# Optimization experiments

Hardware: AMD Instinct MI355X
Metric: run time of the kernel (lower is better)

## Reference

```python
import jax, jax.numpy as jnp
import numpy as np

B, T, H, W = 4, 32, 160, 320
NF, FPF = 8, 8          # num_filters, features_per_filter
SPEED_DIM = 8           # speed_embedding output width
U = 64                  # internal LTC neurons (wiring units)
S = NF * FPF + SPEED_DIM  # 72 sensory inputs
M = 1                   # motor (output) neurons
ODE_UNFOLDS = 6
EPS = 1e-8


def setup_inputs() -> dict:
    key = jax.random.key(0)
    k = jax.random.split(key, 20)
    f32 = jnp.float32
    sp = (H // 8) * (W // 8)  # spatial size per filter after 3 stride-2 convs = 800
    d = {}
    d["input_sequence"] = jax.random.normal(k[0], (B, T, 3, H, W), f32)
    d["speed_sequence"] = jax.random.uniform(k[1], (B, T, 1), f32)
    # conv head params
    d["conv1_w"] = jax.random.normal(k[2], (16, 3, 5, 5), f32) * 0.05
    d["conv1_b"] = jnp.zeros((16,), f32)
    d["conv2_w"] = jax.random.normal(k[3], (32, 16, 5, 5), f32) * 0.05
    d["conv2_b"] = jnp.zeros((32,), f32)
    d["conv3_w"] = jax.random.normal(k[4], (NF, 32, 5, 5), f32) * 0.05
    d["conv3_b"] = jnp.zeros((NF,), f32)
    d["head_w"] = jax.random.normal(k[5], (NF, sp, FPF), f32) * 0.02  # per-filter Linear
    d["head_b"] = jnp.zeros((NF, FPF), f32)
    # speed embedding MLP (Dropout is identity at inference)
    d["se_w1"] = jax.random.normal(k[6], (1, 16), f32) * 0.5
    d["se_b1"] = jnp.zeros((16,), f32)
    d["se_w2"] = jax.random.normal(k[7], (16, SPEED_DIM), f32) * 0.3
    d["se_b2"] = jnp.zeros((SPEED_DIM,), f32)
    # LTC cell params (ncps-style init ranges)
    d["input_w"] = jnp.ones((S,), f32)
    d["input_b"] = jnp.zeros((S,), f32)
    d["gleak"] = jax.random.uniform(k[8], (U,), f32, 0.001, 1.0)
    d["vleak"] = jax.random.uniform(k[9], (U,), f32, -0.2, 0.2)
    d["cm"] = jax.random.uniform(k[10], (U,), f32, 0.4, 0.6)
    d["sigma"] = jax.random.uniform(k[11], (U, U), f32, 3.0, 8.0)
    d["mu"] = jax.random.uniform(k[12], (U, U), f32, 0.3, 0.8)
    d["w_syn"] = jax.random.uniform(k[13], (U, U), f32, 0.001, 1.0)
    d["erev"] = jnp.asarray(jax.random.bernoulli(k[14], 0.5, (U, U)), f32) * 2.0 - 1.0
    d["sensory_sigma"] = jax.random.uniform(k[15], (S, U), f32, 3.0, 8.0)
    d["sensory_mu"] = jax.random.uniform(k[16], (S, U), f32, 0.3, 0.8)
    d["sensory_w"] = jax.random.uniform(k[17], (S, U), f32, 0.001, 1.0)
    d["sensory_erev"] = jnp.asarray(jax.random.bernoulli(k[18], 0.5, (S, U)), f32) * 2.0 - 1.0
    d["output_w"] = jnp.ones((M,), f32)
    d["output_b"] = jnp.zeros((M,), f32)
    return d


def _conv(x, w, b, stride):
    y = jax.lax.conv_general_dilated(
        x, w, (stride, stride), [(2, 2), (2, 2)],
        dimension_numbers=("NCHW", "OIHW", "NCHW"))
    return jax.nn.relu(y + b[None, :, None, None])


def reference(input_sequence, speed_sequence, conv1_w, conv1_b, conv2_w, conv2_b,
              conv3_w, conv3_b, head_w, head_b, se_w1, se_b1, se_w2, se_b2,
              input_w, input_b, gleak, vleak, cm, sigma, mu, w_syn, erev,
              sensory_sigma, sensory_mu, sensory_w, sensory_erev, output_w, output_b):
    Bv, Tv = input_sequence.shape[:2]
    # ---- conv head over all frames at once ----
    x = input_sequence.reshape(Bv * Tv, 3, H, W)
    x = _conv(x, conv1_w, conv1_b, 2)
    x = _conv(x, conv2_w, conv2_b, 2)
    x = _conv(x, conv3_w, conv3_b, 2)          # [N, NF, H/8, W/8]
    x = x.reshape(Bv * Tv, NF, -1)             # [N, NF, 800]
    feats = jnp.einsum("nfp,fpk->nfk", x, head_w) + head_b  # per-filter Linear
    feats = feats.reshape(Bv, Tv, NF * FPF)    # [B, T, 64]
    # global-std normalization (torch .std() uses ddof=1)
    feats = feats / (jnp.std(feats, ddof=1) + 1e-5)
    # ---- speed embedding (vectorized over B,T) ----
    s = speed_sequence[..., :1]                # [B, T, 1]
    emb = jnp.tanh(jax.nn.relu(s @ se_w1 + se_b1) @ se_w2 + se_b2)  # [B, T, 8]
    xs = jnp.concatenate([feats, emb], axis=-1)   # [B, T, S]
    xs = jnp.swapaxes(xs, 0, 1)                   # [T, B, S]
    cm_t = cm * ODE_UNFOLDS  # cm / (elapsed_time / ode_unfolds), elapsed_time = 1.0

    def step(v, x_t):
        inp = x_t * input_w + input_b  # affine input mapping, [B, S]
        s_act = sensory_w * jax.nn.sigmoid((inp[:, :, None] - sensory_mu) * sensory_sigma)  # [B,S,U]
        w_num_s = jnp.sum(s_act * sensory_erev, axis=1)
        w_den_s = jnp.sum(s_act, axis=1)
        for _ in range(ODE_UNFOLDS):  # semi-implicit Euler unfolds
            w_act = w_syn * jax.nn.sigmoid((v[:, :, None] - mu) * sigma)  # [B,U,U]
            w_num = jnp.sum(w_act * erev, axis=1) + w_num_s
            w_den = jnp.sum(w_act, axis=1) + w_den_s
            v = (cm_t * v + gleak * vleak + w_num) / (cm_t + gleak + w_den + EPS)
        out = v[:, :M] * output_w + output_b  # affine output mapping on motor neurons
        return v, (out, v)

    v0 = jnp.zeros((Bv, U), feats.dtype)
    v_last, (outs, hs) = jax.lax.scan(step, v0, xs)
    readout = jnp.swapaxes(outs, 0, 1)  # [B, T, M]
    all_h = jnp.swapaxes(hs, 0, 1)      # [B, T, U]
    return readout, v_last, all_h
```

## Files before the change

kernel.cpp:

```cpp
#include <hip/hip_runtime.h>
#include <math.h>

#define BB 4
#define TT 32
#define NF 8
#define FPF 8
#define SDIM 8
#define UU 64
#define SS 72
#define UNFOLDS 6

typedef short short8 __attribute__((ext_vector_type(8)));
typedef float f32x4 __attribute__((ext_vector_type(4)));
union Frag { uint4 u; short8 s; };

__device__ __forceinline__ float fast_sigmoid(float x) {
    float e = exp2f(-1.44269504f * x);
    return __builtin_amdgcn_rcpf(1.0f + e);
}

__device__ __forceinline__ ushort f2b(float f) {
    union { float f; uint u; } a;
    a.f = f;
    uint u = a.u;
    return (ushort)((u + 0x7FFFu + ((u >> 16) & 1u)) >> 16);
}

__device__ __forceinline__ float bcast_lane(float v, int lane) {
    return __uint_as_float(__builtin_amdgcn_readlane(__float_as_uint(v), lane));
}

__device__ __forceinline__ void cvt_body(const float* __restrict__ in,
                                         ushort* __restrict__ outp, int idx) {
    int x = idx % 320;
    int r = idx / 320;
    int y = r % 160;
    int n = r / 160;
    const float* base = in + ((size_t)n * 3 * 160 + y) * 320 + x;
    float c0 = base[0];
    float c1 = base[160 * 320];
    float c2 = base[2 * 160 * 320];
    uint2 pk;
    pk.x = (uint)f2b(c0) | ((uint)f2b(c1) << 16);
    pk.y = (uint)f2b(c2);
    *(uint2*)(outp + ((size_t)((n * 164 + y + 2) * 328) + (x + 2)) * 4) = pk;
}

template <int HP, int WP, int H, int W, int CH>
__device__ __forceinline__ void halo_body(ushort* __restrict__ buf, int bid) {
    constexpr int TOPBOT = 2 * WP;
    constexpr int SIDE = WP - W;
    constexpr int NH = 2 * TOPBOT + H * SIDE;
    int idx = bid * 256 + threadIdx.x;
    if (idx >= 128 * NH) return;
    int n = idx / NH;
    int h = idx - n * NH;
    int y, x;
    if (h < TOPBOT) {
        y = h / WP;
        x = h % WP;
    } else if (h < 2 * TOPBOT) {
        int hh = h - TOPBOT;
        y = H + 2 + hh / WP;
        x = hh % WP;
    } else {
        int hh = h - 2 * TOPBOT;
        y = 2 + hh / SIDE;
        int xi = hh % SIDE;
        x = (xi < 2) ? xi : (W + xi);
    }
    ushort* p = buf + (((size_t)n * HP + y) * WP + x) * CH;
    if constexpr (CH == 4) {
        *(uint2*)p = make_uint2(0u, 0u);
    } else {
        uint4 z = make_uint4(0u, 0u, 0u, 0u);
#pragma unroll
        for (int i = 0; i < CH / 8; i++) *(uint4*)(p + i * 8) = z;
    }
}

__device__ __forceinline__ uint4 pack8(const ushort v[8]) {
    uint4 u;
    u.x = (uint)v[0] | ((uint)v[1] << 16);
    u.y = (uint)v[2] | ((uint)v[3] << 16);
    u.z = (uint)v[4] | ((uint)v[5] << 16);
    u.w = (uint)v[6] | ((uint)v[7] << 16);
    return u;
}

__device__ __forceinline__ void wswz1_body(const float* __restrict__ w, uint4* __restrict__ o,
                                           int i) {
    int lane = i & 63, s = i >> 6;
    int oc = lane & 15, q = lane >> 4;
    ushort v[8];
#pragma unroll
    for (int j = 0; j < 8; j++) {
        int k = q * 8 + j;
        int kx = k >> 2, c = k & 3;
        float f = (kx < 5 && c < 3) ? w[((oc * 3 + c) * 5 + s) * 5 + kx] : 0.f;
        v[j] = f2b(f);
    }
    o[i] = pack8(v);
}
__device__ __forceinline__ void wswz2_body(const float* __restrict__ w, uint4* __restrict__ o,
                                           int i) {
    int lane = i & 63;
    int ct = (i >> 6) & 1;
    int s = i >> 7;
    int ky = s / 3, kxp = s % 3;
    int oc = ct * 16 + (lane & 15);
    int q = lane >> 4, h = q >> 1;
    int kx = 2 * kxp + h;
    ushort v[8];
#pragma unroll
    for (int j = 0; j < 8; j++) {
        int ch = (q & 1) * 8 + j;
        float f = (kx < 5) ? w[((oc * 16 + ch) * 5 + ky) * 5 + kx] : 0.f;
        v[j] = f2b(f);
    }
    o[i] = pack8(v);
}
__device__ __forceinline__ void wswz3_body(const float* __restrict__ w, uint4* __restrict__ o,
                                           int i) {
    int lane = i & 63, s = i >> 6;
    int ky = s / 5, kx = s % 5;
    int oc = lane & 15, q = lane >> 4;
    ushort v[8];
#pragma unroll
    for (int j = 0; j < 8; j++) {
        int ch = q * 8 + j;
        float f = (oc < 8) ? w[((oc * 32 + ch) * 5 + ky) * 5 + kx] : 0.f;
        v[j] = f2b(f);
    }
    o[i] = pack8(v);
}

__global__ __launch_bounds__(256) void prep_kernel(
    const float* __restrict__ in_seq, ushort* __restrict__ inp1, ushort* __restrict__ c1out,
    ushort* __restrict__ c2out, const float* __restrict__ c1w, const float* __restrict__ c2w,
    const float* __restrict__ c3w, uint4* __restrict__ wz1, uint4* __restrict__ wz2,
    uint4* __restrict__ wz3) {
    int bid = blockIdx.x;
    if (bid < 25600) {
        cvt_body(in_seq, inp1, bid * 256 + threadIdx.x);
    } else if (bid < 25600 + 2032) {
        int hb = bid - 25600;
        if (hb < 1296)
            halo_body<164, 328, 160, 320, 4>(inp1, hb);
        else if (hb < 1296 + 488)
            halo_body<84, 164, 80, 160, 16>(c1out, hb - 1296);
        else
            halo_body<44, 84, 40, 80, 32>(c2out, hb - 1784);
    } else {
        int i = (bid - 27632) * 256 + threadIdx.x;
        if (i < 320)
            wswz1_body(c1w, wz1, i);
        else if (i < 2240)
            wswz2_body(c2w, wz2, i - 320);
        else
            wswz3_body(c3w, wz3, i - 2240);
    }
}

__global__ __launch_bounds__(256) void conv1_mfma(const ushort* __restrict__ inp,
                                                  const uint4* __restrict__ wswz,
                                                  const float* __restrict__ bias,
                                                  ushort* __restrict__ outp) {
    const int lane = threadIdx.x & 63;
    const int wid = threadIdx.x >> 6;
    const int col = lane & 15, q = lane >> 4;

    Frag A[5];
#pragma unroll
    for (int s = 0; s < 5; s++) A[s].u = wswz[s * 64 + lane];
    float b0 = bias[q * 4 + 0], b1 = bias[q * 4 + 1], b2 = bias[q * 4 + 2], b3 = bias[q * 4 + 3];

    int gw = blockIdx.x * 4 + wid;
#pragma unroll
    for (int t = 0; t < 4; t++) {
        int p0 = gw * 64 + t * 16;
        int n = p0 / 12800;
        int rem = p0 - n * 12800;
        int oy = rem / 160;
        int ox0 = rem - oy * 160;
        int ox = ox0 + col;
        uint e0 = ((uint)(n * 164 + oy * 2) * 328u + (uint)(ox * 2 + 2 * q)) * 4u;
        f32x4 acc = {0.f, 0.f, 0.f, 0.f};
#pragma unroll
        for (int s = 0; s < 5; s++) {
            Frag B;
            B.u = *(const uint4*)(inp + e0 + (uint)s * (328u * 4u));
            acc = __builtin_amdgcn_mfma_f32_16x16x32_bf16(A[s].s, B.s, acc, 0, 0, 0);
        }
        uint oe = ((uint)(n * 84 + oy + 2) * 164u + (uint)(ox + 2)) * 16u + q * 4u;
        uint2 pk;
        pk.x = (uint)f2b(fmaxf(acc[0] + b0, 0.f)) | ((uint)f2b(fmaxf(acc[1] + b1, 0.f)) << 16);
        pk.y = (uint)f2b(fmaxf(acc[2] + b2, 0.f)) | ((uint)f2b(fmaxf(acc[3] + b3, 0.f)) << 16);
        *(uint2*)(outp + oe) = pk;
    }
}

__global__ __launch_bounds__(256) void conv2_mfma(const ushort* __restrict__ inp,
                                                  const uint4* __restrict__ wswz,
                                                  const float* __restrict__ bias,
                                                  ushort* __restrict__ outp) {
    const int lane = threadIdx.x & 63;
    const int wid = threadIdx.x >> 6;
    const int col = lane & 15, q = lane >> 4;
    const int h = q >> 1, chh = q & 1;

    int gw = blockIdx.x * 4 + wid;
    uint eb[4];
#pragma unroll
    for (int t = 0; t < 4; t++) {
        int p0 = gw * 64 + t * 16;
        int n = p0 / 3200;
        int rem = p0 - n * 3200;
        int oy = rem / 80;
        int ox0 = rem - oy * 80;
        eb[t] = ((uint)(n * 84 + oy * 2) * 164u + (uint)((ox0 + col) * 2 + h)) * 16u + chh * 8u;
    }
    f32x4 acc[4][2];
#pragma unroll
    for (int t = 0; t < 4; t++) {
        acc[t][0] = {0.f, 0.f, 0.f, 0.f};
        acc[t][1] = {0.f, 0.f, 0.f, 0.f};
    }
#pragma unroll
    for (int s = 0; s < 15; s++) {
        const int ky = s / 3, kxp = s % 3;
        Frag A0, A1;
        A0.u = wswz[(s * 2 + 0) * 64 + lane];
        A1.u = wswz[(s * 2 + 1) * 64 + lane];
        const uint d = (uint)ky * (164u * 16u) + (uint)kxp * 32u;
#pragma unroll
        for (int t = 0; t < 4; t++) {
            Frag B;
            B.u = *(const uint4*)(inp + eb[t] + d);
            acc[t][0] = __builtin_amdgcn_mfma_f32_16x16x32_bf16(A0.s, B.s, acc[t][0], 0, 0, 0);
            acc[t][1] = __builtin_amdgcn_mfma_f32_16x16x32_bf16(A1.s, B.s, acc[t][1], 0, 0, 0);
        }
    }
    float ba[2][4];
#pragma unroll
    for (int c = 0; c < 2; c++)
#pragma unroll
        for (int r = 0; r < 4; r++) ba[c][r] = bias[c * 16 + q * 4 + r];
#pragma unroll
    for (int t = 0; t < 4; t++) {
        int p0 = gw * 64 + t * 16;
        int n = p0 / 3200;
        int rem = p0 - n * 3200;
        int oy = rem / 80;
        int ox0 = rem - oy * 80;
        int ox = ox0 + col;
        uint oe = ((uint)(n * 44 + oy + 2) * 84u + (uint)(ox + 2)) * 32u;
#pragma unroll
        for (int c = 0; c < 2; c++) {
            uint2 pk;
            pk.x = (uint)f2b(fmaxf(acc[t][c][0] + ba[c][0], 0.f)) |
                   ((uint)f2b(fmaxf(acc[t][c][1] + ba[c][1], 0.f)) << 16);
            pk.y = (uint)f2b(fmaxf(acc[t][c][2] + ba[c][2], 0.f)) |
                   ((uint)f2b(fmaxf(acc[t][c][3] + ba[c][3], 0.f)) << 16);
            *(uint2*)(outp + oe + (uint)c * 16u + (uint)q * 4u) = pk;
        }
    }
}

__global__ __launch_bounds__(256) void conv3_mfma(const ushort* __restrict__ inp,
                                                  const uint4* __restrict__ wswz,
                                                  const float* __restrict__ bias,
                                                  float* __restrict__ outp) {
    const int lane = threadIdx.x & 63;
    const int wid = threadIdx.x >> 6;
    const int col = lane & 15, q = lane >> 4;

    int gw = blockIdx.x * 4 + wid;
    uint eb[4];
#pragma unroll
    for (int t = 0; t < 4; t++) {
        int p0 = gw * 64 + t * 16;
        int n = p0 / 800;
        int pix = p0 - n * 800 + col;
        int oy = pix / 40;
        int ox = pix - oy * 40;
        eb[t] = ((uint)(n * 44 + oy * 2) * 84u + (uint)(ox * 2)) * 32u + q * 8u;
    }
    f32x4 acc[4];
#pragma unroll
    for (int t = 0; t < 4; t++) acc[t] = {0.f, 0.f, 0.f, 0.f};
#pragma unroll
    for (int s = 0; s < 25; s++) {
        const int ky = s / 5, kx = s % 5;
        Frag A;
        A.u = wswz[s * 64 + lane];
        const uint d = ((uint)ky * 84u + (uint)kx) * 32u;
#pragma unroll
        for (int t = 0; t < 4; t++) {
            Frag B;
            B.u = *(const uint4*)(inp + eb[t] + d);
            acc[t] = __builtin_amdgcn_mfma_f32_16x16x32_bf16(A.s, B.s, acc[t], 0, 0, 0);
        }
    }
    if (q < 2) {
        float b0 = bias[q * 4 + 0], b1 = bias[q * 4 + 1];
        float b2 = bias[q * 4 + 2], b3 = bias[q * 4 + 3];
#pragma unroll
        for (int t = 0; t < 4; t++) {
            int p0 = gw * 64 + t * 16;
            int n = p0 / 800;
            int p = p0 - n * 800 + col;
            float4 v;
            v.x = fmaxf(acc[t][0] + b0, 0.f);
            v.y = fmaxf(acc[t][1] + b1, 0.f);
            v.z = fmaxf(acc[t][2] + b2, 0.f);
            v.w = fmaxf(acc[t][3] + b3, 0.f);
            *(float4*)(outp + ((size_t)n * 800 + p) * 8 + q * 4) = v;
        }
    }
}

__global__ __launch_bounds__(256) void head_kernel(const float* __restrict__ x,
                                                   const float* __restrict__ hw,
                                                   const float* __restrict__ hb,
                                                   float* __restrict__ feats) {
    __shared__ float part[4][64];
    int n = blockIdx.x;
    int tid = threadIdx.x;
    int lane = tid & 63;
    int c = tid >> 6;
    int f = lane >> 3;
    int k = lane & 7;
    const float* xb = x + (size_t)n * 800 * 8 + f;
    const float* wb = hw + ((size_t)f * 800) * FPF + k;
    float acc = 0.0f;
    for (int p = c * 200; p < c * 200 + 200; p++)
        acc = fmaf(xb[(size_t)p * 8], wb[(size_t)p * FPF], acc);
    part[c][lane] = acc;
    __syncthreads();
    if (c == 0)
        feats[n * 64 + lane] = part[0][lane] + part[1][lane] + part[2][lane] + part[3][lane] +
                               hb[lane];
}

__global__ __launch_bounds__(512, 1) void scan_fused(
    const float* __restrict__ feats, const float* __restrict__ speed,
    const float* __restrict__ sew1, const float* __restrict__ seb1,
    const float* __restrict__ sew2, const float* __restrict__ seb2,
    const float* __restrict__ inw, const float* __restrict__ inb,
    const float* __restrict__ ssig, const float* __restrict__ smu,
    const float* __restrict__ sw, const float* __restrict__ serev,
    const float* __restrict__ gleak, const float* __restrict__ vleak,
    const float* __restrict__ cm, const float* __restrict__ sigma,
    const float* __restrict__ mu, const float* __restrict__ wsyn,
    const float* __restrict__ erev, const float* __restrict__ outw,
    const float* __restrict__ outb, float* __restrict__ dout) {
    int b = blockIdx.x;
    int tid = threadIdx.x;
    int u = tid & 63;
    int pc_s = __builtin_amdgcn_readfirstlane(tid >> 6);

    __shared__ float2 red[512];
    __shared__ float2 sens[TT][UU];
    __shared__ float embsh[TT][SDIM];
    __shared__ float2 pbuf[2][8][64];

    float sA[8], sB[8], wer[8], w_[8];
#pragma unroll
    for (int i = 0; i < 8; i++) {
        int idx = (pc_s * 8 + i) * UU + u;
        float sg = sigma[idx];
        sA[i] = -1.44269504f * sg;
        sB[i] = -sA[i] * mu[idx];
        w_[i] = wsyn[idx];
        wer[i] = w_[i] * erev[idx];
    }
#pragma unroll
    for (int i = 0; i < 8; i++) {
        asm volatile("" : "+v"(sA[i]), "+v"(sB[i]), "+v"(wer[i]), "+v"(w_[i]));
    }

    float s = 0.0f, q = 0.0f;
    for (int i = tid; i < 8192; i += 512) {
        float x = feats[i];
        s += x;
        q += x * x;
    }
    red[tid] = make_float2(s, q);
    __syncthreads();
    for (int off = 256; off > 0; off >>= 1) {
        if (tid < off) {
            float2 o = red[tid + off];
            float2 m = red[tid];
            red[tid] = make_float2(m.x + o.x, m.y + o.y);
        }
        __syncthreads();
    }
    float2 SQ = red[0];
    float mean = SQ.x / 8192.0f;
    float var = fmaxf((SQ.y - 8192.0f * mean * mean) / 8191.0f, 0.0f);
    float inv = 1.0f / (sqrtf(var) + 1e-5f);

    if (tid < 256) {
        int t = tid >> 3, k = tid & 7;
        float sp = speed[b * TT + t];
        float a = seb2[k];
#pragma unroll
        for (int j = 0; j < 16; j++) {
            float h = fmaxf(fmaf(sp, sew1[j], seb1[j]), 0.0f);
            a = fmaf(h, sew2[j * SDIM + k], a);
        }
        embsh[t][k] = tanhf(a);
    }
    __syncthreads();

#pragma unroll
    for (int p = 0; p < 4; p++) {
        int pair = p * 512 + tid;
        int t = pair >> 6;
        int uu = pair & 63;
        int n = b * TT + t;
        float num = 0.0f, den = 0.0f;
        for (int ss = 0; ss < SS; ss++) {
            float xsv = (ss < 64) ? feats[n * 64 + ss] * inv : embsh[t][ss - 64];
            float inp = fmaf(xsv, inw[ss], inb[ss]);
            int idx = ss * UU + uu;
            float x = (inp - smu[idx]) * ssig[idx];
            float act = sw[idx] * fast_sigmoid(x);
            num = fmaf(act, serev[idx], num);
            den += act;
        }
        sens[t][uu] = make_float2(num, den);
    }
    __syncthreads();

    float cmt = cm[u] * (float)UNFOLDS;
    float gl = gleak[u];
    float glvl = gl * vleak[u];
    float ow = outw[0], ob = outb[0];
    float v = 0.0f;
    int par = 0;

    for (int t = 0; t < TT; t++) {
        float2 nsd = sens[t][u];
        float num_s = nsd.x, den_s = nsd.y;
#pragma unroll
        for (int k = 0; k < UNFOLDS; k++) {
            float num = 0.0f, den = 0.0f;
#pragma unroll
            for (int i = 0; i < 8; i++) {
                float vi = bcast_lane(v, pc_s * 8 + i);
                float e = exp2f(fmaf(vi, sA[i], sB[i]));
                float r = __builtin_amdgcn_rcpf(1.0f + e);
                num = fmaf(wer[i], r, num);
                den = fmaf(w_[i], r, den);
            }
            pbuf[par][pc_s][u] = make_float2(num, den);
            __builtin_amdgcn_sched_barrier(0);
            asm volatile("s_waitcnt lgkmcnt(0)" ::: "memory");
            __builtin_amdgcn_s_barrier();
            asm volatile("" ::: "memory");
            __builtin_amdgcn_sched_barrier(0);
            float nn = num_s, dd = den_s;
#pragma unroll
            for (int j = 0; j < 8; j++) {
                float2 p = pbuf[par][j][u];
                nn += p.x;
                dd += p.y;
            }
            float denom = cmt + gl + dd + 1e-8f;
            v = (fmaf(cmt, v, glvl) + nn) * __builtin_amdgcn_rcpf(denom);
            par ^= 1;
        }
        if (pc_s == 0) {
            dout[384 + (b * TT + t) * UU + u] = v;
            if (u == 0) dout[b * TT + t] = fmaf(v, ow, ob);
            if (t == TT - 1) dout[128 + b * UU + u] = v;
        }
    }
}

extern "C" void kernel_launch(void* const* d_in, const int* in_sizes, int n_in,
                              void* d_out, int out_size, void* d_ws, size_t ws_size,
                              hipStream_t stream) {
    const float* in_seq = (const float*)d_in[0];
    const float* speed = (const float*)d_in[1];
    const float* c1w = (const float*)d_in[2];
    const float* c1b = (const float*)d_in[3];
    const float* c2w = (const float*)d_in[4];
    const float* c2b = (const float*)d_in[5];
    const float* c3w = (const float*)d_in[6];
    const float* c3b = (const float*)d_in[7];
    const float* hw = (const float*)d_in[8];
    const float* hb = (const float*)d_in[9];
    const float* sew1 = (const float*)d_in[10];
    const float* seb1 = (const float*)d_in[11];
    const float* sew2 = (const float*)d_in[12];
    const float* seb2 = (const float*)d_in[13];
    const float* inw = (const float*)d_in[14];
    const float* inb = (const float*)d_in[15];
    const float* gleak = (const float*)d_in[16];
    const float* vleak = (const float*)d_in[17];
    const float* cm = (const float*)d_in[18];
    const float* sigma = (const float*)d_in[19];
    const float* mu = (const float*)d_in[20];
    const float* wsyn = (const float*)d_in[21];
    const float* erev = (const float*)d_in[22];
    const float* ssig = (const float*)d_in[23];
    const float* smu = (const float*)d_in[24];
    const float* sw = (const float*)d_in[25];
    const float* serev = (const float*)d_in[26];
    const float* outw = (const float*)d_in[27];
    const float* outb = (const float*)d_in[28];

    char* ws = (char*)d_ws;
    float* out = (float*)d_out;

    size_t off = 0;
    auto alloc = [&](size_t bytes) {
        size_t o = off;
        off += (bytes + 255) & ~(size_t)255;
        return o;
    };
    ushort* inp1 = (ushort*)(ws + alloc((size_t)128 * 164 * 328 * 4 * 2));
    ushort* c1out = (ushort*)(ws + alloc((size_t)128 * 84 * 164 * 16 * 2));
    ushort* c2out = (ushort*)(ws + alloc((size_t)128 * 44 * 84 * 32 * 2));
    float* c3out = (float*)(ws + alloc((size_t)128 * 800 * 8 * 4));
    float* feats = (float*)(ws + alloc(8192 * 4));
    uint4* wz1 = (uint4*)(ws + alloc(5 * 64 * 16));
    uint4* wz2 = (uint4*)(ws + alloc(30 * 64 * 16));
    uint4* wz3 = (uint4*)(ws + alloc(25 * 64 * 16));

    prep_kernel<<<27647, 256, 0, stream>>>(in_seq, inp1, c1out, c2out, c1w, c2w, c3w, wz1,
                                           wz2, wz3);

    conv1_mfma<<<6400, 256, 0, stream>>>(inp1, wz1, c1b, c1out);
    conv2_mfma<<<1600, 256, 0, stream>>>(c1out, wz2, c2b, c2out);
    conv3_mfma<<<400, 256, 0, stream>>>(c2out, wz3, c3b, c3out);

    head_kernel<<<128, 256, 0, stream>>>(c3out, hw, hb, feats);

    scan_fused<<<BB, 512, 0, stream>>>(feats, speed, sew1, seb1, sew2, seb2, inw, inb, ssig,
                                       smu, sw, serev, gleak, vleak, cm, sigma, mu, wsyn,
                                       erev, outw, outb, out);
}
```

Measured before the change: 301.0 us.

## Fuse conv pipeline into persistent megakernel with grid barriers, parallelize sensory precompute

Replaces the separate prep, conv1-3 and head launches with one persistent kernel of 1024 blocks that loops over virtual blocks and separates stages with atomic-counter grid barriers. The feature normalization statistics and the sensory synapse sums move out of the 4-block scan kernel into 128 parallel blocks, and the scan kernel only prefetches the precomputed per-step values. The aim is to remove launch gaps and the serial prologue of the scan. The cost is spin-wait barrier overhead, a memset launch, and reliance on all 1024 blocks being co-resident, which could deadlock if occupancy is insufficient.

Measured after the change: 1.049 ms. +248.5%, slower.

```diff
diff --git a/kernel.cpp b/kernel.cpp
--- a/kernel.cpp
+++ b/kernel.cpp
@@ -9,6 +9,7 @@
 #define UU 64
 #define SS 72
 #define UNFOLDS 6
+#define GRID 1024
 
 typedef short short8 __attribute__((ext_vector_type(8)));
 typedef float f32x4 __attribute__((ext_vector_type(4)));
@@ -28,6 +29,19 @@
 
 __device__ __forceinline__ float bcast_lane(float v, int lane) {
     return __uint_as_float(__builtin_amdgcn_readlane(__float_as_uint(v), lane));
+}
+
+__device__ __forceinline__ void gsync(uint* cnt, uint target) {
+    __syncthreads();
+    if (threadIdx.x == 0) {
+        __threadfence();
+        __hip_atomic_fetch_add(cnt, 1u, __ATOMIC_ACQ_REL, __HIP_MEMORY_SCOPE_AGENT);
+        while (__hip_atomic_load(cnt, __ATOMIC_RELAXED, __HIP_MEMORY_SCOPE_AGENT) < target) {
+            __builtin_amdgcn_s_sleep(8);
+        }
+        __threadfence();
+    }
+    __syncthreads();
 }
 
 __device__ __forceinline__ void cvt_body(const float* __restrict__ in,
@@ -135,47 +149,18 @@
     o[i] = pack8(v);
 }
 
-__global__ __launch_bounds__(256) void prep_kernel(
-    const float* __restrict__ in_seq, ushort* __restrict__ inp1, ushort* __restrict__ c1out,
-    ushort* __restrict__ c2out, const float* __restrict__ c1w, const float* __restrict__ c2w,
-    const float* __restrict__ c3w, uint4* __restrict__ wz1, uint4* __restrict__ wz2,
-    uint4* __restrict__ wz3) {
-    int bid = blockIdx.x;
-    if (bid < 25600) {
-        cvt_body(in_seq, inp1, bid * 256 + threadIdx.x);
-    } else if (bid < 25600 + 2032) {
-        int hb = bid - 25600;
-        if (hb < 1296)
-            halo_body<164, 328, 160, 320, 4>(inp1, hb);
-        else if (hb < 1296 + 488)
-            halo_body<84, 164, 80, 160, 16>(c1out, hb - 1296);
-        else
-            halo_body<44, 84, 40, 80, 32>(c2out, hb - 1784);
-    } else {
-        int i = (bid - 27632) * 256 + threadIdx.x;
-        if (i < 320)
-            wswz1_body(c1w, wz1, i);
-        else if (i < 2240)
-            wswz2_body(c2w, wz2, i - 320);
-        else
-            wswz3_body(c3w, wz3, i - 2240);
-    }
-}
-
-__global__ __launch_bounds__(256) void conv1_mfma(const ushort* __restrict__ inp,
-                                                  const uint4* __restrict__ wswz,
-                                                  const float* __restrict__ bias,
-                                                  ushort* __restrict__ outp) {
+__device__ __forceinline__ void conv1_body(int gw4, const ushort* __restrict__ inp,
+                                           const uint4* __restrict__ wswz,
+                                           const float* __restrict__ bias,
+                                           ushort* __restrict__ outp) {
     const int lane = threadIdx.x & 63;
     const int wid = threadIdx.x >> 6;
     const int col = lane & 15, q = lane >> 4;
-
     Frag A[5];
 #pragma unroll
     for (int s = 0; s < 5; s++) A[s].u = wswz[s * 64 + lane];
     float b0 = bias[q * 4 + 0], b1 = bias[q * 4 + 1], b2 = bias[q * 4 + 2], b3 = bias[q * 4 + 3];
-
-    int gw = blockIdx.x * 4 + wid;
+    int gw = gw4 * 4 + wid;
 #pragma unroll
     for (int t = 0; t < 4; t++) {
         int p0 = gw * 64 + t * 16;
@@ -200,16 +185,15 @@
     }
 }
 
-__global__ __launch_bounds__(256) void conv2_mfma(const ushort* __restrict__ inp,
-                                                  const uint4* __restrict__ wswz,
-                                                  const float* __restrict__ bias,
-                                                  ushort* __restrict__ outp) {
+__device__ __forceinline__ void conv2_body(int gw4, const ushort* __restrict__ inp,
+                                           const uint4* __restrict__ wswz,
+                                           const float* __restrict__ bias,
+                                           ushort* __restrict__ outp) {
     const int lane = threadIdx.x & 63;
     const int wid = threadIdx.x >> 6;
     const int col = lane & 15, q = lane >> 4;
     const int h = q >> 1, chh = q & 1;
-
-    int gw = blockIdx.x * 4 + wid;
+    int gw = gw4 * 4 + wid;
     uint eb[4];
 #pragma unroll
     for (int t = 0; t < 4; t++) {
@@ -267,15 +251,14 @@
     }
 }
 
-__global__ __launch_bounds__(256) void conv3_mfma(const ushort* __restrict__ inp,
-                                                  const uint4* __restrict__ wswz,
-                                                  const float* __restrict__ bias,
-                                                  float* __restrict__ outp) {
+__device__ __forceinline__ void conv3_body(int gw4, const ushort* __restrict__ inp,
+                                           const uint4* __restrict__ wswz,
+                                           const float* __restrict__ bias,
+                                           float* __restrict__ outp) {
     const int lane = threadIdx.x & 63;
     const int wid = threadIdx.x >> 6;
     const int col = lane & 15, q = lane >> 4;
-
-    int gw = blockIdx.x * 4 + wid;
+    int gw = gw4 * 4 + wid;
     uint eb[4];
 #pragma unroll
     for (int t = 0; t < 4; t++) {
@@ -320,36 +303,131 @@
     }
 }
 
-__global__ __launch_bounds__(256) void head_kernel(const float* __restrict__ x,
-                                                   const float* __restrict__ hw,
-                                                   const float* __restrict__ hb,
-                                                   float* __restrict__ feats) {
-    __shared__ float part[4][64];
-    int n = blockIdx.x;
-    int tid = threadIdx.x;
-    int lane = tid & 63;
-    int c = tid >> 6;
-    int f = lane >> 3;
-    int k = lane & 7;
-    const float* xb = x + (size_t)n * 800 * 8 + f;
-    const float* wb = hw + ((size_t)f * 800) * FPF + k;
-    float acc = 0.0f;
-    for (int p = c * 200; p < c * 200 + 200; p++)
-        acc = fmaf(xb[(size_t)p * 8], wb[(size_t)p * FPF], acc);
-    part[c][lane] = acc;
-    __syncthreads();
-    if (c == 0)
-        feats[n * 64 + lane] = part[0][lane] + part[1][lane] + part[2][lane] + part[3][lane] +
-                               hb[lane];
-}
-
-__global__ __launch_bounds__(512, 1) void scan_fused(
-    const float* __restrict__ feats, const float* __restrict__ speed,
+__global__ __launch_bounds__(256, 4) void mega_shell(
+    const float* __restrict__ in_seq, const float* __restrict__ speed,
+    const float* __restrict__ c1w, const float* __restrict__ c1b,
+    const float* __restrict__ c2w, const float* __restrict__ c2b,
+    const float* __restrict__ c3w, const float* __restrict__ c3b,
+    const float* __restrict__ hw, const float* __restrict__ hb,
     const float* __restrict__ sew1, const float* __restrict__ seb1,
     const float* __restrict__ sew2, const float* __restrict__ seb2,
     const float* __restrict__ inw, const float* __restrict__ inb,
     const float* __restrict__ ssig, const float* __restrict__ smu,
     const float* __restrict__ sw, const float* __restrict__ serev,
+    ushort* __restrict__ inp1, ushort* __restrict__ c1out, ushort* __restrict__ c2out,
+    float* __restrict__ c3out, float* __restrict__ feats, float* __restrict__ emb,
+    float* __restrict__ wns, float* __restrict__ wds, uint4* __restrict__ wz1,
+    uint4* __restrict__ wz2, uint4* __restrict__ wz3, uint* __restrict__ bar,
+    double* __restrict__ dacc) {
+    const int bid = blockIdx.x;
+    const int tid = threadIdx.x;
+    __shared__ float part[4][64];
+
+    for (int vb = bid; vb < 27647; vb += GRID) {
+        if (vb < 25600) {
+            cvt_body(in_seq, inp1, vb * 256 + tid);
+        } else if (vb < 27632) {
+            int hb = vb - 25600;
+            if (hb < 1296)
+                halo_body<164, 328, 160, 320, 4>(inp1, hb);
+            else if (hb < 1784)
+                halo_body<84, 164, 80, 160, 16>(c1out, hb - 1296);
+            else
+                halo_body<44, 84, 40, 80, 32>(c2out, hb - 1784);
+        } else {
+            int i = (vb - 27632) * 256 + tid;
+            if (i < 320)
+                wswz1_body(c1w, wz1, i);
+            else if (i < 2240)
+                wswz2_body(c2w, wz2, i - 320);
+            else
+                wswz3_body(c3w, wz3, i - 2240);
+        }
+    }
+    if (bid == GRID - 1 && tid < 128) {
+        float sp = speed[tid];
+        float h[16];
+#pragma unroll
+        for (int j = 0; j < 16; j++) h[j] = fmaxf(fmaf(sp, sew1[j], seb1[j]), 0.0f);
+#pragma unroll
+        for (int k = 0; k < SDIM; k++) {
+            float a = seb2[k];
+#pragma unroll
+            for (int j = 0; j < 16; j++) a = fmaf(h[j], sew2[j * SDIM + k], a);
+            emb[tid * SDIM + k] = tanhf(a);
+        }
+    }
+    gsync(bar, 1 * GRID);
+
+    for (int vb = bid; vb < 6400; vb += GRID) conv1_body(vb, inp1, wz1, c1b, c1out);
+    gsync(bar, 2 * GRID);
+
+    for (int vb = bid; vb < 1600; vb += GRID) conv2_body(vb, c1out, wz2, c2b, c2out);
+    gsync(bar, 3 * GRID);
+
+    for (int vb = bid; vb < 400; vb += GRID) conv3_body(vb, c2out, wz3, c3b, c3out);
+    gsync(bar, 4 * GRID);
+
+    for (int vb = bid; vb < 128; vb += GRID) {
+        int lane = tid & 63;
+        int c = tid >> 6;
+        int f = lane >> 3;
+        int k = lane & 7;
+        const float* xb = c3out + (size_t)vb * 800 * 8 + f;
+        const float* wb = hw + ((size_t)f * 800) * FPF + k;
+        float acc = 0.0f;
+        for (int p = c * 200; p < c * 200 + 200; p++)
+            acc = fmaf(xb[(size_t)p * 8], wb[(size_t)p * FPF], acc);
+        part[c][lane] = acc;
+        __syncthreads();
+        if (c == 0)
+            feats[vb * 64 + lane] =
+                part[0][lane] + part[1][lane] + part[2][lane] + part[3][lane] + hb[lane];
+        __syncthreads();
+    }
+    gsync(bar, 5 * GRID);
+
+    if (bid < 128 && tid < 64) {
+        float x = feats[bid * 64 + tid];
+        float s = x, q = x * x;
+#pragma unroll
+        for (int off = 32; off > 0; off >>= 1) {
+            s += __shfl_down(s, off);
+            q += __shfl_down(q, off);
+        }
+        if (tid == 0) {
+            atomicAdd(&dacc[0], (double)s);
+            atomicAdd(&dacc[1], (double)q);
+        }
+    }
+    gsync(bar, 6 * GRID);
+
+    if (bid < 128 && tid < 64) {
+        double S = dacc[0], Q = dacc[1];
+        float mean = (float)(S / 8192.0);
+        float var = fmaxf((float)((Q - 8192.0 * (double)mean * (double)mean) / 8191.0), 0.0f);
+        float inv = 1.0f / (sqrtf(var) + 1e-5f);
+        int t = bid >> 2;
+        int b = bid & 3;
+        int u = tid;
+        int n = b * TT + t;
+        float num = 0.0f, den = 0.0f;
+        for (int s = 0; s < SS; s++) {
+            float xsv = (s < 64) ? feats[n * 64 + s] * inv : emb[n * SDIM + (s - 64)];
+            float inp = fmaf(xsv, inw[s], inb[s]);
+            int idx = s * UU + u;
+            float x = (inp - smu[idx]) * ssig[idx];
+            float act = sw[idx] * fast_sigmoid(x);
+            num = fmaf(act, serev[idx], num);
+            den += act;
+        }
+        wns[bid * UU + u] = num;
+        wds[bid * UU + u] = den;
+    }
+}
+
+__global__ __launch_bounds__(512, 1) void scan_kernel(
+    const float* __restrict__ wns, const float* __restrict__ wds,
     const float* __restrict__ gleak, const float* __restrict__ vleak,
     const float* __restrict__ cm, const float* __restrict__ sigma,
     const float* __restrict__ mu, const float* __restrict__ wsyn,
@@ -360,9 +438,6 @@
     int u = tid & 63;
     int pc_s = __builtin_amdgcn_readfirstlane(tid >> 6);
 
-    __shared__ float2 red[512];
-    __shared__ float2 sens[TT][UU];
-    __shared__ float embsh[TT][SDIM];
     __shared__ float2 pbuf[2][8][64];
 
     float sA[8], sB[8], wer[8], w_[8];
@@ -379,61 +454,6 @@
     for (int i = 0; i < 8; i++) {
         asm volatile("" : "+v"(sA[i]), "+v"(sB[i]), "+v"(wer[i]), "+v"(w_[i]));
     }
-
-    float s = 0.0f, q = 0.0f;
-    for (int i = tid; i < 8192; i += 512) {
-        float x = feats[i];
-        s += x;
-        q += x * x;
-    }
-    red[tid] = make_float2(s, q);
-    __syncthreads();
-    for (int off = 256; off > 0; off >>= 1) {
-        if (tid < off) {
-            float2 o = red[tid + off];
-            float2 m = red[tid];
-            red[tid] = make_float2(m.x + o.x, m.y + o.y);
-        }
-        __syncthreads();
-    }
-    float2 SQ = red[0];
-    float mean = SQ.x / 8192.0f;
-    float var = fmaxf((SQ.y - 8192.0f * mean * mean) / 8191.0f, 0.0f);
-    float inv = 1.0f / (sqrtf(var) + 1e-5f);
-
-    if (tid < 256) {
-        int t = tid >> 3, k = tid & 7;
-        float sp = speed[b * TT + t];
-        float a = seb2[k];
-#pragma unroll
-        for (int j = 0; j < 16; j++) {
-            float h = fmaxf(fmaf(sp, sew1[j], seb1[j]), 0.0f);
-            a = fmaf(h, sew2[j * SDIM + k], a);
-        }
-        embsh[t][k] = tanhf(a);
-    }
-    __syncthreads();
-
-#pragma unroll
-    for (int p = 0; p < 4; p++) {
-        int pair = p * 512 + tid;
-        int t = pair >> 6;
-        int uu = pair & 63;
-        int n = b * TT + t;
-        float num = 0.0f, den = 0.0f;
-        for (int ss = 0; ss < SS; ss++) {
-            float xsv = (ss < 64) ? feats[n * 64 + ss] * inv : embsh[t][ss - 64];
-            float inp = fmaf(xsv, inw[ss], inb[ss]);
-            int idx = ss * UU + uu;
-            float x = (inp - smu[idx]) * ssig[idx];
-            float act = sw[idx] * fast_sigmoid(x);
-            num = fmaf(act, serev[idx], num);
-            den += act;
-        }
-        sens[t][uu] = make_float2(num, den);
-    }
-    __syncthreads();
-
     float cmt = cm[u] * (float)UNFOLDS;
     float gl = gleak[u];
     float glvl = gl * vleak[u];
@@ -441,9 +461,14 @@
     float v = 0.0f;
     int par = 0;
 
+    float num_s = wns[(0 * BB + b) * UU + u];
+    float den_s = wds[(0 * BB + b) * UU + u];
     for (int t = 0; t < TT; t++) {
-        float2 nsd = sens[t][u];
-        float num_s = nsd.x, den_s = nsd.y;
+        float nns = 0.f, nds = 0.f;
+        if (t + 1 < TT) {
+            nns = wns[((t + 1) * BB + b) * UU + u];
+            nds = wds[((t + 1) * BB + b) * UU + u];
+        }
 #pragma unroll
         for (int k = 0; k < UNFOLDS; k++) {
             float num = 0.0f, den = 0.0f;
@@ -477,6 +502,8 @@
             if (u == 0) dout[b * TT + t] = fmaf(v, ow, ob);
             if (t == TT - 1) dout[128 + b * UU + u] = v;
         }
+        num_s = nns;
+        den_s = nds;
     }
 }
 
@@ -527,20 +554,23 @@
     ushort* c2out = (ushort*)(ws + alloc((size_t)128 * 44 * 84 * 32 * 2));
     float* c3out = (float*)(ws + alloc((size_t)128 * 800 * 8 * 4));
     float* feats = (float*)(ws + alloc(8192 * 4));
+    float* emb = (float*)(ws + alloc(1024 * 4));
+    float* wns = (float*)(ws + alloc(8192 * 4));
+    float* wds = (float*)(ws + alloc(8192 * 4));
     uint4* wz1 = (uint4*)(ws + alloc(5 * 64 * 16));
     uint4* wz2 = (uint4*)(ws + alloc(30 * 64 * 16));
     uint4* wz3 = (uint4*)(ws + alloc(25 * 64 * 16));
-
-    prep_kernel<<<27647, 256, 0, stream>>>(in_seq, inp1, c1out, c2out, c1w, c2w, c3w, wz1,
-                                           wz2, wz3);
-
-    conv1_mfma<<<6400, 256, 0, stream>>>(inp1, wz1, c1b, c1out);
-    conv2_mfma<<<1600, 256, 0, stream>>>(c1out, wz2, c2b, c2out);
-    conv3_mfma<<<400, 256, 0, stream>>>(c2out, wz3, c3b, c3out);
-
-    head_kernel<<<128, 256, 0, stream>>>(c3out, hw, hb, feats);
-
-    scan_fused<<<BB, 512, 0, stream>>>(feats, speed, sew1, seb1, sew2, seb2, inw, inb, ssig,
-                                       smu, sw, serev, gleak, vleak, cm, sigma, mu, wsyn,
-                                       erev, outw, outb, out);
-}
+    char* barrier_area = ws + alloc(64);
+    uint* bar = (uint*)barrier_area;
+    double* dacc = (double*)(barrier_area + 16);
+
+    hipMemsetAsync(barrier_area, 0, 64, stream);
+
+    mega_shell<<<GRID, 256, 0, stream>>>(in_seq, speed, c1w, c1b, c2w, c2b, c3w, c3b, hw, hb,
+                                         sew1, seb1, sew2, seb2, inw, inb, ssig, smu, sw,
+                                         serev, inp1, c1out, c2out, c3out, feats, emb, wns,
+                                         wds, wz1, wz2, wz3, bar, dacc);
+
+    scan_kernel<<<BB, 512, 0, stream>>>(wns, wds, gleak, vleak, cm, sigma, mu, wsyn, erev,
+                                        outw, outb, out);
+}
```

## Split sensory precompute into a separate wide kernel before the LTC scan

Applied to the files above, without the earlier changes.

Moves the feature normalization, speed embedding and sensory synapse sums out of the 4-block scan kernel into a new 128-block kernel, one block per (t,b). This spreads that work across many CUs instead of serializing it on 4 blocks ahead of the recurrence. The scan kernel then reads the precomputed sums from global memory, prefetching the next timestep's values. The cost is an extra kernel launch, redundant global-stats reduction in every block, and a global round trip for the sensory sums.

New measurement: 285.0 us. -5.3%, faster.

```diff
diff --git a/kernel.cpp b/kernel.cpp
--- a/kernel.cpp
+++ b/kernel.cpp
@@ -343,13 +343,64 @@
                                hb[lane];
 }
 
-__global__ __launch_bounds__(512, 1) void scan_fused(
+__global__ __launch_bounds__(64) void sensory_semb(
     const float* __restrict__ feats, const float* __restrict__ speed,
     const float* __restrict__ sew1, const float* __restrict__ seb1,
     const float* __restrict__ sew2, const float* __restrict__ seb2,
     const float* __restrict__ inw, const float* __restrict__ inb,
     const float* __restrict__ ssig, const float* __restrict__ smu,
     const float* __restrict__ sw, const float* __restrict__ serev,
+    float* __restrict__ wns, float* __restrict__ wds) {
+    int bid = blockIdx.x;
+    int t = bid >> 2;
+    int b = bid & 3;
+    int u = threadIdx.x;
+    int n = b * TT + t;
+
+    float s = 0.0f, q = 0.0f;
+    for (int i = u; i < 8192; i += 64) {
+        float x = feats[i];
+        s += x;
+        q += x * x;
+    }
+#pragma unroll
+    for (int off = 32; off > 0; off >>= 1) {
+        s += __shfl_xor(s, off);
+        q += __shfl_xor(q, off);
+    }
+    float mean = s / 8192.0f;
+    float var = fmaxf((q - 8192.0f * mean * mean) / 8191.0f, 0.0f);
+    float inv = 1.0f / (sqrtf(var) + 1e-5f);
+
+    float sp = speed[n];
+    float h[16];
+#pragma unroll
+    for (int j = 0; j < 16; j++) h[j] = fmaxf(fmaf(sp, sew1[j], seb1[j]), 0.0f);
+    float embv[SDIM];
+#pragma unroll
+    for (int k = 0; k < SDIM; k++) {
+        float a = seb2[k];
+#pragma unroll
+        for (int j = 0; j < 16; j++) a = fmaf(h[j], sew2[j * SDIM + k], a);
+        embv[k] = tanhf(a);
+    }
+
+    float num = 0.0f, den = 0.0f;
+    for (int ss = 0; ss < SS; ss++) {
+        float xsv = (ss < 64) ? feats[n * 64 + ss] * inv : embv[ss - 64];
+        float inp = fmaf(xsv, inw[ss], inb[ss]);
+        int idx = ss * UU + u;
+        float x = (inp - smu[idx]) * ssig[idx];
+        float act = sw[idx] * fast_sigmoid(x);
+        num = fmaf(act, serev[idx], num);
+        den += act;
+    }
+    wns[bid * UU + u] = num;
+    wds[bid * UU + u] = den;
+}
+
+__global__ __launch_bounds__(512, 1) void scan_kernel(
+    const float* __restrict__ wns, const float* __restrict__ wds,
     const float* __restrict__ gleak, const float* __restrict__ vleak,
     const float* __restrict__ cm, const float* __restrict__ sigma,
     const float* __restrict__ mu, const float* __restrict__ wsyn,
@@ -360,9 +411,6 @@
     int u = tid & 63;
     int pc_s = __builtin_amdgcn_readfirstlane(tid >> 6);
 
-    __shared__ float2 red[512];
-    __shared__ float2 sens[TT][UU];
-    __shared__ float embsh[TT][SDIM];
     __shared__ float2 pbuf[2][8][64];
 
     float sA[8], sB[8], wer[8], w_[8];
@@ -379,61 +427,6 @@
     for (int i = 0; i < 8; i++) {
         asm volatile("" : "+v"(sA[i]), "+v"(sB[i]), "+v"(wer[i]), "+v"(w_[i]));
     }
-
-    float s = 0.0f, q = 0.0f;
-    for (int i = tid; i < 8192; i += 512) {
-        float x = feats[i];
-        s += x;
-        q += x * x;
-    }
-    red[tid] = make_float2(s, q);
-    __syncthreads();
-    for (int off = 256; off > 0; off >>= 1) {
-        if (tid < off) {
-            float2 o = red[tid + off];
-            float2 m = red[tid];
-            red[tid] = make_float2(m.x + o.x, m.y + o.y);
-        }
-        __syncthreads();
-    }
-    float2 SQ = red[0];
-    float mean = SQ.x / 8192.0f;
-    float var = fmaxf((SQ.y - 8192.0f * mean * mean) / 8191.0f, 0.0f);
-    float inv = 1.0f / (sqrtf(var) + 1e-5f);
-
-    if (tid < 256) {
-        int t = tid >> 3, k = tid & 7;
-        float sp = speed[b * TT + t];
-        float a = seb2[k];
-#pragma unroll
-        for (int j = 0; j < 16; j++) {
-            float h = fmaxf(fmaf(sp, sew1[j], seb1[j]), 0.0f);
-            a = fmaf(h, sew2[j * SDIM + k], a);
-        }
-        embsh[t][k] = tanhf(a);
-    }
-    __syncthreads();
-
-#pragma unroll
-    for (int p = 0; p < 4; p++) {
-        int pair = p * 512 + tid;
-        int t = pair >> 6;
-        int uu = pair & 63;
-        int n = b * TT + t;
-        float num = 0.0f, den = 0.0f;
-        for (int ss = 0; ss < SS; ss++) {
-            float xsv = (ss < 64) ? feats[n * 64 + ss] * inv : embsh[t][ss - 64];
-            float inp = fmaf(xsv, inw[ss], inb[ss]);
-            int idx = ss * UU + uu;
-            float x = (inp - smu[idx]) * ssig[idx];
-            float act = sw[idx] * fast_sigmoid(x);
-            num = fmaf(act, serev[idx], num);
-            den += act;
-        }
-        sens[t][uu] = make_float2(num, den);
-    }
-    __syncthreads();
-
     float cmt = cm[u] * (float)UNFOLDS;
     float gl = gleak[u];
     float glvl = gl * vleak[u];
@@ -441,9 +434,14 @@
     float v = 0.0f;
     int par = 0;
 
+    float num_s = wns[(0 * BB + b) * UU + u];
+    float den_s = wds[(0 * BB + b) * UU + u];
     for (int t = 0; t < TT; t++) {
-        float2 nsd = sens[t][u];
-        float num_s = nsd.x, den_s = nsd.y;
+        float nns = 0.f, nds = 0.f;
+        if (t + 1 < TT) {
+            nns = wns[((t + 1) * BB + b) * UU + u];
+            nds = wds[((t + 1) * BB + b) * UU + u];
+        }
 #pragma unroll
         for (int k = 0; k < UNFOLDS; k++) {
             float num = 0.0f, den = 0.0f;
@@ -477,6 +475,8 @@
             if (u == 0) dout[b * TT + t] = fmaf(v, ow, ob);
             if (t == TT - 1) dout[128 + b * UU + u] = v;
         }
+        num_s = nns;
+        den_s = nds;
     }
 }
 
@@ -527,6 +527,8 @@
     ushort* c2out = (ushort*)(ws + alloc((size_t)128 * 44 * 84 * 32 * 2));
     float* c3out = (float*)(ws + alloc((size_t)128 * 800 * 8 * 4));
     float* feats = (float*)(ws + alloc(8192 * 4));
+    float* wns = (float*)(ws + alloc(8192 * 4));
+    float* wds = (float*)(ws + alloc(8192 * 4));
     uint4* wz1 = (uint4*)(ws + alloc(5 * 64 * 16));
     uint4* wz2 = (uint4*)(ws + alloc(30 * 64 * 16));
     uint4* wz3 = (uint4*)(ws + alloc(25 * 64 * 16));
@@ -540,7 +542,9 @@
 
     head_kernel<<<128, 256, 0, stream>>>(c3out, hw, hb, feats);
 
-    scan_fused<<<BB, 512, 0, stream>>>(feats, speed, sew1, seb1, sew2, seb2, inw, inb, ssig,
-                                       smu, sw, serev, gleak, vleak, cm, sigma, mu, wsyn,
-                                       erev, outw, outb, out);
-}
+    sensory_semb<<<128, 64, 0, stream>>>(feats, speed, sew1, seb1, sew2, seb2, inw, inb,
+                                         ssig, smu, sw, serev, wns, wds);
+
+    scan_kernel<<<BB, 512, 0, stream>>>(wns, wds, gleak, vleak, cm, sigma, mu, wsyn, erev,
+                                        outw, outb, out);
+}
```
